# Kernel optimization log

Measured on AMD Instinct MI355X. Metric: run time of the kernel, lower is better.

## Reference

```python
import jax, jax.numpy as jnp
import numpy as np

T, K, N = 4096, 4096, 11008  # tokens, in_features, out_features


def _unpack_int4(packed):
    """packed: int8 [..., K//2] -> signed 4-bit values int8 [..., K].
    Low nibble first, high nibble second; arithmetic shifts sign-extend."""
    lo = jnp.right_shift(jnp.left_shift(packed, 4).astype(jnp.int8), 4)
    hi = jnp.right_shift(packed, 4).astype(jnp.int8)
    out = jnp.stack([lo, hi], axis=-1)  # [..., K//2, 2]
    return out.reshape(*packed.shape[:-1], packed.shape[-1] * 2)


def _pack_int4(vals):
    """vals: int8 in [-8,7], [..., K] -> packed int8 [..., K//2]."""
    v = vals.reshape(*vals.shape[:-1], vals.shape[-1] // 2, 2)
    lo = v[..., 0] & 0xF
    hi = v[..., 1] & 0xF
    return (lo | jnp.left_shift(hi, 4)).astype(jnp.int8)


def setup_inputs() -> dict:
    key = jax.random.key(0)
    k1, k2, k3, k4 = jax.random.split(key, 4)
    # symmetric 4-bit quantized values in [-7, 7], packed two per byte
    x_int = jax.random.randint(k1, (T, K), -7, 8).astype(jnp.int8)
    w_int = jax.random.randint(k2, (N, K), -7, 8).astype(jnp.int8)
    pq_x = _pack_int4(x_int)
    weight = _pack_int4(w_int)
    # per-token / per-output-channel dequant scales (max_abs/7 style magnitudes)
    scales_x = (jax.random.uniform(k3, (T,), jnp.float32) * 0.01 + 1e-4)
    weight_scales = (jax.random.uniform(k4, (N,), jnp.float32) * 0.01 + 1e-4)
    return {"pq_x": pq_x, "scales_x": scales_x, "weight": weight,
            "weight_scales": weight_scales}


def reference(pq_x, scales_x, weight, weight_scales):
    # Unpack int4 operands. Products |a*w| <= 49 and K=4096 => |acc| <= 2e5,
    # exactly representable in fp32, so the fp32 matmul equals int32 GEMM.
    a = _unpack_int4(pq_x).astype(jnp.float32)      # [T, K]
    w = _unpack_int4(weight).astype(jnp.float32)    # [N, K]
    acc = jnp.einsum('tk,nk->tn', a, w)             # integer GEMM in fp32
    # fused per-token x per-output-channel dequant
    out = acc * scales_x[:, None] * weight_scales[None, :]
    out = out.astype(jnp.float16)
    return out[None]  # unsqueeze(0) as in the torch module
```

## Files before the change

### kernel.cpp

```cpp
#include <hip/hip_runtime.h>
#include <hip/hip_fp16.h>
#include <stdint.h>


#define T_DIM 4096
#define K_DIM 4096
#define N_DIM 11008
#define KP    2048
#define BM 128
#define BN 256
#define STAGES 64
#define A_PANELS (T_DIM / BM)
#define B_PANELS (N_DIM / BN)
#define CHUNK_A 8192
#define CHUNK_B 16384
#define WS_A ((size_t)A_PANELS * STAGES * CHUNK_A)
#define WS_B ((size_t)B_PANELS * STAGES * CHUNK_B)
#define NA_BYTES ((size_t)T_DIM * KP)
#define NW_BYTES ((size_t)N_DIM * KP)

typedef __attribute__((ext_vector_type(4)))  int int32x4;
typedef __attribute__((ext_vector_type(16))) int int32x16;
typedef __attribute__((ext_vector_type(4)))  float floatx4;
typedef __attribute__((ext_vector_type(8)))  _Float16 f16x8;
typedef __attribute__((ext_vector_type(2)))  _Float16 f16x2;

__device__ __forceinline__ uint32_t pack4(int4 v) {
  return (uint32_t)(v.x & 0xFF) | ((uint32_t)(v.y & 0xFF) << 8) |
         ((uint32_t)(v.z & 0xFF) << 16) | ((uint32_t)(v.w & 0xFF) << 24);
}
__device__ __forceinline__ uint32_t nib_lo_s8(uint32_t p) {
  uint32_t t = (p & 0x0F0F0F0Fu) ^ 0x88888888u;
  return (t - 0x08080808u) ^ 0x80808080u;
}
__device__ __forceinline__ uint32_t nib_hi_s8(uint32_t p) {
  uint32_t t = ((p >> 4) & 0x0F0F0F0Fu) ^ 0x88888888u;
  return (t - 0x08080808u) ^ 0x80808080u;
}

__global__ __launch_bounds__(256) void unpack_tiles2(
    const int* __restrict__ xa, const int* __restrict__ xw,
    uint8_t* __restrict__ wsa, uint8_t* __restrict__ wsb)
{
  const int s  = blockIdx.x;
  const int yb = blockIdx.y;
  const int t  = threadIdx.x;
  const int r  = t >> 1, h = t & 1;

  const int* src; uint8_t* dst; int cellStride;
  if (yb < A_PANELS) {
    src = xa + ((size_t)(yb * 128 + r)) * KP + s * 32 + h * 16;
    dst = wsa + ((size_t)yb * STAGES + s) * CHUNK_A + r * 16;
    cellStride = 2048;
  } else {
    const int yb2 = yb - A_PANELS;
    const int panel = yb2 >> 1;
    const int rip = (yb2 & 1) * 128 + r;
    src = xw + ((size_t)(yb2 * 128 + r)) * KP + s * 32 + h * 16;
    dst = wsb + ((size_t)panel * STAGES + s) * CHUNK_B + rip * 16;
    cellStride = 4096;
  }
  const int4* s4 = (const int4*)src;
  const int4 v0 = s4[0], v1 = s4[1], v2 = s4[2], v3 = s4[3];
  const uint32_t b0 = pack4(v0), b1 = pack4(v1);
  const uint32_t b2 = pack4(v2), b3 = pack4(v3);
  uint4 o01, o23;
  o01.x = nib_lo_s8(b0); o01.y = nib_hi_s8(b0);
  o01.z = nib_lo_s8(b1); o01.w = nib_hi_s8(b1);
  o23.x = nib_lo_s8(b2); o23.y = nib_hi_s8(b2);
  o23.z = nib_lo_s8(b3); o23.w = nib_hi_s8(b3);
  *(uint4*)(dst + (2 * h    ) * cellStride) = o01;
  *(uint4*)(dst + (2 * h + 1) * cellStride) = o23;
}

__device__ __forceinline__ void dma16(const uint8_t* g, uint8_t* l) {
  __builtin_amdgcn_global_load_lds(
      (const __attribute__((address_space(1))) uint32_t*)g,
      (__attribute__((address_space(3))) uint32_t*)l, 16, 0, 0);
}

__global__ __launch_bounds__(256, 2) void gemm_i8_db(
    const uint8_t* __restrict__ wsa, const uint8_t* __restrict__ wsb,
    const float* __restrict__ sx, const float* __restrict__ sw,
    float* __restrict__ out)
{
  __shared__ uint8_t sA[2][CHUNK_A];
  __shared__ uint8_t sB[2][CHUNK_B];

  const int tid  = threadIdx.x;
  const int lane = tid & 63;
  const int wv   = tid >> 6;
  const int wm   = wv >> 1, wn = wv & 1;
  const int h    = lane >> 5;
  const int ml   = lane & 31;
  const int pp   = blockIdx.x;
  const int qq   = blockIdx.y;

  const uint8_t* chunkA = wsa + (size_t)pp * STAGES * CHUNK_A;
  const uint8_t* chunkB = wsb + (size_t)qq * STAGES * CHUNK_B;
  const int segOff = wv * 1024 + lane * 16;
  const int ldsOff = wv * 1024;

  const int rowA = (wm * 64 + ml) * 16;
  const int rowB = (wn * 128 + ml) * 16;

  int32x16 acc[2][4];
#pragma unroll
  for (int mi = 0; mi < 2; ++mi)
#pragma unroll
    for (int ni = 0; ni < 4; ++ni)
#pragma unroll
      for (int i = 0; i < 16; ++i) acc[mi][ni][i] = 0;

  auto dma_stage = [&](int s, int buf) {
    const uint8_t* ca = chunkA + (size_t)s * CHUNK_A;
    const uint8_t* cb = chunkB + (size_t)s * CHUNK_B;
#pragma unroll
    for (int i = 0; i < 2; ++i)
      dma16(ca + segOff + i * 4096, &sA[buf][ldsOff + i * 4096]);
#pragma unroll
    for (int i = 0; i < 4; ++i)
      dma16(cb + segOff + i * 4096, &sB[buf][ldsOff + i * 4096]);
  };

  dma_stage(0, 0);

#pragma unroll 1
  for (int s = 0; s < STAGES; ++s) {
    const int buf = s & 1;
    __syncthreads();
    if (s + 1 < STAGES) dma_stage(s + 1, buf ^ 1);
#pragma unroll
    for (int s2 = 0; s2 < 2; ++s2) {
      const int c = 2 * s2 + h;
      const uint8_t* pa = &sA[buf][c * 2048 + rowA];
      const uint8_t* pb = &sB[buf][c * 4096 + rowB];
      int32x4 aF[2], bF[4];
#pragma unroll
      for (int mi = 0; mi < 2; ++mi) aF[mi] = *(const int32x4*)(pa + mi * 512);
#pragma unroll
      for (int ni = 0; ni < 4; ++ni) bF[ni] = *(const int32x4*)(pb + ni * 512);
#pragma unroll
      for (int mi = 0; mi < 2; ++mi)
#pragma unroll
        for (int ni = 0; ni < 4; ++ni)
          acc[mi][ni] = __builtin_amdgcn_mfma_i32_32x32x32_i8(
              aF[mi], bF[ni], acc[mi][ni], 0, 0, 0);
    }
  }

#pragma unroll
  for (int mi = 0; mi < 2; ++mi) {
    const int rb = pp * BM + wm * 64 + mi * 32 + 4 * h;
    float sxv[16];
#pragma unroll
    for (int r = 0; r < 16; ++r) sxv[r] = sx[rb + (r & 3) + 8 * (r >> 2)];
#pragma unroll
    for (int ni = 0; ni < 4; ++ni) {
      const int gcol = qq * BN + wn * 128 + ni * 32 + ml;
      const float swv = sw[gcol];
#pragma unroll
      for (int r = 0; r < 16; ++r) {
        const int grow = rb + (r & 3) + 8 * (r >> 2);
        const float v = (float)acc[mi][ni][r] * sxv[r] * swv;
        out[(size_t)grow * N_DIM + gcol] = __half2float(__float2half(v));
      }
    }
  }
}

__global__ __launch_bounds__(256) void repack_int32_to_bytes(
    const int* __restrict__ xa, const int* __restrict__ xw,
    uint32_t* __restrict__ da, uint32_t* __restrict__ dw)
{
  const size_t i = (size_t)blockIdx.x * blockDim.x + threadIdx.x;
  const size_t na4 = NA_BYTES / 4;
  const int4* src; uint32_t* dst; size_t off;
  if (i < na4) { src = (const int4*)xa; dst = da; off = i; }
  else         { src = (const int4*)xw; dst = dw; off = i - na4; }
  const int4 v = src[off];
  dst[off] = pack4(v);
}

__device__ __forceinline__ uint32_t cvt2(uint32_t m) {
  union U { uint32_t u; f16x2 h; } a, b, c;
  a.u = m ^ 0x64086408u; b.u = 0xE408E408u; c.h = a.h + b.h;
  return c.u;
}
__device__ __forceinline__ void unpack_cell(uint32_t* cell, uint32_t p) {
  cell[0] = cvt2( p        & 0x000F000Fu);
  cell[1] = cvt2((p >> 4)  & 0x000F000Fu);
  cell[2] = cvt2((p >> 8)  & 0x000F000Fu);
  cell[3] = cvt2((p >> 12) & 0x000F000Fu);
}

template <bool PACKED>
__global__ __launch_bounds__(256) void linear4bit_f16(
    const uint8_t* __restrict__ pqx, const float* __restrict__ sx,
    const uint8_t* __restrict__ wq,  const float* __restrict__ sw,
    const int* __restrict__ pqx32,   const int* __restrict__ wq32,
    float* __restrict__ out)
{
  __shared__ uint32_t sAf[8][128][4];
  __shared__ uint32_t sBf[8][128][4];
  const int tid = threadIdx.x, lane = tid & 63, wv = tid >> 6;
  const int wm = wv >> 1, wn = wv & 1, qd = lane >> 4, m16 = lane & 15;
  const int bm0 = blockIdx.x * 128, bn0 = blockIdx.y * 128;
  const int srow = tid >> 1, sh = tid & 1;
  const uint8_t* aPtr = pqx + (size_t)(bm0 + srow) * KP + sh * 16;
  const uint8_t* bPtr = wq  + (size_t)(bn0 + srow) * KP + sh * 16;
  const int* aPtr32 = pqx32 + (size_t)(bm0 + srow) * KP + sh * 16;
  const int* bPtr32 = wq32  + (size_t)(bn0 + srow) * KP + sh * 16;
  floatx4 acc[4][4];
#pragma unroll
  for (int mi = 0; mi < 4; ++mi)
#pragma unroll
    for (int ni = 0; ni < 4; ++ni)
#pragma unroll
      for (int r = 0; r < 4; ++r) acc[mi][ni][r] = 0.0f;
  uint4 ar, br;
  auto load_stage = [&](int s) {
    if (PACKED) {
      ar = *(const uint4*)(aPtr + (size_t)s * 32);
      br = *(const uint4*)(bPtr + (size_t)s * 32);
    } else {
      const int4* a4 = (const int4*)(aPtr32 + (size_t)s * 32);
      const int4* b4 = (const int4*)(bPtr32 + (size_t)s * 32);
      ar.x = pack4(a4[0]); ar.y = pack4(a4[1]); ar.z = pack4(a4[2]); ar.w = pack4(a4[3]);
      br.x = pack4(b4[0]); br.y = pack4(b4[1]); br.z = pack4(b4[2]); br.w = pack4(b4[3]);
    }
  };
  auto stage_to_lds = [&]() {
    uint32_t pa[4] = {ar.x, ar.y, ar.z, ar.w};
    uint32_t pb[4] = {br.x, br.y, br.z, br.w};
#pragma unroll
    for (int i = 0; i < 4; ++i) {
      unpack_cell(&sAf[4 * sh + i][srow][0], pa[i]);
      unpack_cell(&sBf[4 * sh + i][srow][0], pb[i]);
    }
  };
  load_stage(0); stage_to_lds();
#pragma unroll 1
  for (int s = 0; s < STAGES; ++s) {
    __syncthreads();
    if (s + 1 < STAGES) load_stage(s + 1);
#pragma unroll
    for (int s2 = 0; s2 < 2; ++s2) {
      f16x8 aF[4], bF[4];
#pragma unroll
      for (int mi = 0; mi < 4; ++mi)
        aF[mi] = *(const f16x8*)&sAf[4 * s2 + qd][wm * 64 + mi * 16 + m16][0];
#pragma unroll
      for (int ni = 0; ni < 4; ++ni)
        bF[ni] = *(const f16x8*)&sBf[4 * s2 + qd][wn * 64 + ni * 16 + m16][0];
#pragma unroll
      for (int mi = 0; mi < 4; ++mi)
#pragma unroll
        for (int ni = 0; ni < 4; ++ni)
          acc[mi][ni] = __builtin_amdgcn_mfma_f32_16x16x32_f16(aF[mi], bF[ni], acc[mi][ni], 0, 0, 0);
    }
    __syncthreads();
    if (s + 1 < STAGES) stage_to_lds();
  }
#pragma unroll
  for (int mi = 0; mi < 4; ++mi) {
    const int grow0 = bm0 + wm * 64 + mi * 16 + qd * 4;
    const float s0 = sx[grow0], s1 = sx[grow0 + 1], s2v = sx[grow0 + 2], s3 = sx[grow0 + 3];
#pragma unroll
    for (int ni = 0; ni < 4; ++ni) {
      const int gcol = bn0 + wn * 64 + ni * 16 + m16;
      const float swv = sw[gcol];
      const floatx4 a = acc[mi][ni];
      out[(size_t)(grow0 + 0) * N_DIM + gcol] = __half2float(__float2half(a[0] * s0 * swv));
      out[(size_t)(grow0 + 1) * N_DIM + gcol] = __half2float(__float2half(a[1] * s1 * swv));
      out[(size_t)(grow0 + 2) * N_DIM + gcol] = __half2float(__float2half(a[2] * s2v * swv));
      out[(size_t)(grow0 + 3) * N_DIM + gcol] = __half2float(__float2half(a[3] * s3 * swv));
    }
  }
}

extern "C" void kernel_launch(void* const* d_in, const int* in_sizes, int n_in,
                              void* d_out, int out_size, void* d_ws, size_t ws_size,
                              hipStream_t stream) {
  const int*   pqx32 = (const int*)d_in[0];
  const float* sxp   = (const float*)d_in[1];
  const int*   wq32  = (const int*)d_in[2];
  const float* swp   = (const float*)d_in[3];
  float* outp = (float*)d_out;

  if (ws_size >= WS_A + WS_B) {
    uint8_t* wsa = (uint8_t*)d_ws;
    uint8_t* wsb = wsa + WS_A;
    unpack_tiles2<<<dim3(STAGES, A_PANELS + N_DIM / 128), 256, 0, stream>>>(
        pqx32, wq32, wsa, wsb);
    gemm_i8_db<<<dim3(A_PANELS, B_PANELS), 256, 0, stream>>>(wsa, wsb, sxp, swp, outp);
  } else if (ws_size >= NA_BYTES + NW_BYTES) {
    uint8_t* da = (uint8_t*)d_ws;
    uint8_t* dw = da + NA_BYTES;
    const size_t total4 = (NA_BYTES + NW_BYTES) / 4;
    repack_int32_to_bytes<<<(uint32_t)(total4 / 256), 256, 0, stream>>>(
        pqx32, wq32, (uint32_t*)da, (uint32_t*)dw);
    linear4bit_f16<true><<<dim3(T_DIM / 128, N_DIM / 128), 256, 0, stream>>>(
        da, sxp, dw, swp, nullptr, nullptr, outp);
  } else {
    linear4bit_f16<false><<<dim3(T_DIM / 128, N_DIM / 128), 256, 0, stream>>>(
        nullptr, sxp, nullptr, swp, pqx32, wq32, outp);
  }
}
```

Measured before the change: 477.7 us.

## Triple-buffer LDS stages with explicit vmcnt waits in int8 GEMM

Moves the int8 MFMA GEMM from double to triple buffering of the LDS staging areas and prefetches two stages ahead. A raw s_barrier guarded by a manual s_waitcnt vmcnt(6) replaces __syncthreads, so one stage of global-to-LDS DMA can stay in flight while the current stage is computed. LDS use grows from 48KB to 72KB per block, which may conflict with the two-blocks-per-CU launch bound and lower occupancy. It also relies on the vmcnt count exactly matching the six DMA ops issued per stage.

```diff
diff --git a/kernel.cpp b/kernel.cpp
--- a/kernel.cpp
+++ b/kernel.cpp
@@ -79,13 +79,13 @@
       (__attribute__((address_space(3))) uint32_t*)l, 16, 0, 0);
 }
 
-__global__ __launch_bounds__(256, 2) void gemm_i8_db(
+__global__ __launch_bounds__(256, 2) void gemm_i8_tb(
     const uint8_t* __restrict__ wsa, const uint8_t* __restrict__ wsb,
     const float* __restrict__ sx, const float* __restrict__ sw,
     float* __restrict__ out)
 {
-  __shared__ uint8_t sA[2][CHUNK_A];
-  __shared__ uint8_t sB[2][CHUNK_B];
+  __shared__ uint8_t sAmem[3 * CHUNK_A];
+  __shared__ uint8_t sBmem[3 * CHUNK_B];
 
   const int tid  = threadIdx.x;
   const int lane = tid & 63;
@@ -115,26 +115,35 @@
   auto dma_stage = [&](int s, int buf) {
     const uint8_t* ca = chunkA + (size_t)s * CHUNK_A;
     const uint8_t* cb = chunkB + (size_t)s * CHUNK_B;
+    uint8_t* la = sAmem + buf * CHUNK_A + ldsOff;
+    uint8_t* lb = sBmem + buf * CHUNK_B + ldsOff;
 #pragma unroll
     for (int i = 0; i < 2; ++i)
-      dma16(ca + segOff + i * 4096, &sA[buf][ldsOff + i * 4096]);
+      dma16(ca + segOff + i * 4096, la + i * 4096);
 #pragma unroll
     for (int i = 0; i < 4; ++i)
-      dma16(cb + segOff + i * 4096, &sB[buf][ldsOff + i * 4096]);
+      dma16(cb + segOff + i * 4096, lb + i * 4096);
   };
 
   dma_stage(0, 0);
-
+  dma_stage(1, 1);
+
+  int rb = 0;
+  int wb = 2;
 #pragma unroll 1
   for (int s = 0; s < STAGES; ++s) {
-    const int buf = s & 1;
-    __syncthreads();
-    if (s + 1 < STAGES) dma_stage(s + 1, buf ^ 1);
+    if (s < STAGES - 1) asm volatile("s_waitcnt vmcnt(6)" ::: "memory");
+    else                asm volatile("s_waitcnt vmcnt(0)" ::: "memory");
+    __builtin_amdgcn_s_barrier();
+    if (s + 2 < STAGES) dma_stage(s + 2, wb);
+
+    const uint8_t* baseA = sAmem + rb * CHUNK_A;
+    const uint8_t* baseB = sBmem + rb * CHUNK_B;
 #pragma unroll
     for (int s2 = 0; s2 < 2; ++s2) {
       const int c = 2 * s2 + h;
-      const uint8_t* pa = &sA[buf][c * 2048 + rowA];
-      const uint8_t* pb = &sB[buf][c * 4096 + rowB];
+      const uint8_t* pa = baseA + c * 2048 + rowA;
+      const uint8_t* pb = baseB + c * 4096 + rowB;
       int32x4 aF[2], bF[4];
 #pragma unroll
       for (int mi = 0; mi < 2; ++mi) aF[mi] = *(const int32x4*)(pa + mi * 512);
@@ -147,21 +156,23 @@
           acc[mi][ni] = __builtin_amdgcn_mfma_i32_32x32x32_i8(
               aF[mi], bF[ni], acc[mi][ni], 0, 0, 0);
     }
+    rb = (rb == 2) ? 0 : rb + 1;
+    wb = (wb == 2) ? 0 : wb + 1;
   }
 
 #pragma unroll
   for (int mi = 0; mi < 2; ++mi) {
-    const int rb = pp * BM + wm * 64 + mi * 32 + 4 * h;
+    const int rbase = pp * BM + wm * 64 + mi * 32 + 4 * h;
     float sxv[16];
 #pragma unroll
-    for (int r = 0; r < 16; ++r) sxv[r] = sx[rb + (r & 3) + 8 * (r >> 2)];
+    for (int r = 0; r < 16; ++r) sxv[r] = sx[rbase + (r & 3) + 8 * (r >> 2)];
 #pragma unroll
     for (int ni = 0; ni < 4; ++ni) {
       const int gcol = qq * BN + wn * 128 + ni * 32 + ml;
       const float swv = sw[gcol];
 #pragma unroll
       for (int r = 0; r < 16; ++r) {
-        const int grow = rb + (r & 3) + 8 * (r >> 2);
+        const int grow = rbase + (r & 3) + 8 * (r >> 2);
         const float v = (float)acc[mi][ni][r] * sxv[r] * swv;
         out[(size_t)grow * N_DIM + gcol] = __half2float(__float2half(v));
       }
@@ -293,7 +304,7 @@
     uint8_t* wsb = wsa + WS_A;
     unpack_tiles2<<<dim3(STAGES, A_PANELS + N_DIM / 128), 256, 0, stream>>>(
         pqx32, wq32, wsa, wsb);
-    gemm_i8_db<<<dim3(A_PANELS, B_PANELS), 256, 0, stream>>>(wsa, wsb, sxp, swp, outp);
+    gemm_i8_tb<<<dim3(A_PANELS, B_PANELS), 256, 0, stream>>>(wsa, wsb, sxp, swp, outp);
   } else if (ws_size >= NA_BYTES + NW_BYTES) {
     uint8_t* da = (uint8_t*)d_ws;
     uint8_t* dw = da + NA_BYTES;
```

Result: no change. 477.1 us (-0.1%).
